# Kernel optimization log

Hardware: AMD Instinct MI355X
Metric: run time of the kernel (lower is better)

The kernel has to match this reference:

```python
import jax, jax.numpy as jnp
import numpy as np

C, H, D = 64, 2, 32
NQ, NA, NE, F_IN = 8192, 32768, 500000, 128
E_E2Q, E_E2E, E_E2A, E_Q2A = 131072, 800000, 262144, 32768
N_POS, N_NEG = 8192, 24576
# node types: 0=question, 1=answer, 2=entity
# edge types (src_type, dst_type): e2q=(2,0), e2e=(2,2), e2a=(2,1), q2a=(0,1)
REL_ST = [(2, 0), (2, 2), (2, 1), (0, 1)]


def _edges(k, n_src, n_dst, e):
    k1, k2 = jax.random.split(k)
    return jnp.stack([jax.random.randint(k1, (e,), 0, n_src),
                      jax.random.randint(k2, (e,), 0, n_dst)]).astype(jnp.int32)


def setup_inputs():
    key = jax.random.key(0)
    ks = jax.random.split(key, 16)
    inp = {
        'x_question': jax.random.normal(ks[0], (NQ, F_IN), jnp.float32),
        'x_answer': jax.random.normal(ks[1], (NA, F_IN), jnp.float32),
        'x_entity': jax.random.normal(ks[2], (NE, F_IN), jnp.float32),
        'e_e2q': _edges(ks[3], NE, NQ, E_E2Q),
        'e_e2e': _edges(ks[4], NE, NE, E_E2E),
        'e_e2a': _edges(ks[5], NE, NA, E_E2A),
        'e_q2a': _edges(ks[6], NQ, NA, E_Q2A),
        'pos_idx': _edges(ks[7], NQ, NA, N_POS),
        'neg_idx': _edges(ks[8], NQ, NA, N_NEG),
        # learned parameters (stacked over the 3 node types / 4 edge types)
        'W_in': jax.random.normal(ks[9], (3, F_IN, C), jnp.float32) / np.sqrt(F_IN).astype(np.float32),
        'b_in': jnp.zeros((3, C), jnp.float32),
        'bn_gamma': jnp.ones((3, C), jnp.float32),
        'bn_beta': jnp.zeros((3, C), jnp.float32),
        'W_kqv': jax.random.normal(ks[10], (3, C, 3 * C), jnp.float32) / np.sqrt(C).astype(np.float32),
        'b_kqv': jnp.zeros((3, 3 * C), jnp.float32),
        'A_k': jax.random.normal(ks[11], (4, H, D, D), jnp.float32) / np.sqrt(D).astype(np.float32),
        'A_v': jax.random.normal(ks[12], (4, H, D, D), jnp.float32) / np.sqrt(D).astype(np.float32),
        'p_rel': jnp.ones((4, H), jnp.float32),
        'W_out': jax.random.normal(ks[13], (3, C, C), jnp.float32) / np.sqrt(C).astype(np.float32),
        'b_out': jnp.zeros((3, C), jnp.float32),
        'skip': jnp.ones((3,), jnp.float32),
    }
    return inp


def _segment_attn(scores, vals, dst, n):
    # scores [E,H], vals [E,H,D]: softmax over incoming edges per dst node, weighted scatter-add
    m = jax.ops.segment_max(scores, dst, num_segments=n)          # [N,H]
    e = jnp.exp(scores - m[dst])                                   # [E,H]
    s = jax.ops.segment_sum(e, dst, num_segments=n)                # [N,H]
    w = e / s[dst]
    return jax.ops.segment_sum(vals * w[..., None], dst, num_segments=n)  # [N,H,D]


def _forward(x_question, x_answer, x_entity, W_in, b_in, bn_gamma, bn_beta,
             W_kqv, b_kqv, A_k, A_v, p_rel, W_out, b_out, skip, edges):
    xs = [x_question, x_answer, x_entity]
    h = []
    for t in range(3):
        y = jax.nn.relu(xs[t] @ W_in[t] + b_in[t])
        mu = y.mean(0)
        var = y.var(0)  # biased, as in torch BN training mode
        y = bn_gamma[t] * (y - mu) * jax.lax.rsqrt(var + 1e-5) + bn_beta[t]
        h.append(y)
    kqv = [h[t] @ W_kqv[t] + b_kqv[t] for t in range(3)]
    k = [kv[:, :C].reshape(-1, H, D) for kv in kqv]
    q = [kv[:, C:2 * C].reshape(-1, H, D) for kv in kqv]
    v = [kv[:, 2 * C:].reshape(-1, H, D) for kv in kqv]
    by_dst = {0: [], 1: [], 2: []}
    inv_sqrt_d = jnp.float32(1.0 / np.sqrt(D))
    for r, ((st, dt), ei) in enumerate(zip(REL_ST, edges)):
        src, dst = ei[0], ei[1]
        k_r = jnp.einsum('ehd,hdf->ehf', k[st][src], A_k[r])   # per-relation key transform
        v_r = jnp.einsum('ehd,hdf->ehf', v[st][src], A_v[r])   # per-relation value transform
        sc = (q[dt][dst] * k_r).sum(-1) * p_rel[r] * inv_sqrt_d  # [E,H]
        by_dst[dt].append((sc, v_r, dst))
    out = []
    for t in range(3):
        sc = jnp.concatenate([a for a, _, _ in by_dst[t]], axis=0)
        vr = jnp.concatenate([b for _, b, _ in by_dst[t]], axis=0)
        dst = jnp.concatenate([c for _, _, c in by_dst[t]], axis=0)
        n = h[t].shape[0]
        agg = _segment_attn(sc, vr, dst, n).reshape(n, C)
        a = jax.nn.gelu(agg, approximate=False) @ W_out[t] + b_out[t]
        g = jax.nn.sigmoid(skip[t])
        out.append(g * a + (1.0 - g) * h[t])
    return out  # [z_question, z_answer, z_entity]


def reference(x_question, x_answer, x_entity, e_e2q, e_e2e, e_e2a, e_q2a,
              pos_idx, neg_idx, W_in, b_in, bn_gamma, bn_beta, W_kqv, b_kqv,
              A_k, A_v, p_rel, W_out, b_out, skip):
    zq, za, ze = _forward(x_question, x_answer, x_entity, W_in, b_in, bn_gamma,
                          bn_beta, W_kqv, b_kqv, A_k, A_v, p_rel, W_out, b_out,
                          skip, [e_e2q, e_e2e, e_e2a, e_q2a])
    pos_pred = (zq[pos_idx[0]] * za[pos_idx[1]]).sum(-1)
    neg_pred = (zq[neg_idx[0]] * za[neg_idx[1]]).sum(-1)
    return pos_pred, neg_pred, zq, za, ze
```

## Files before the change

### kernel.cpp

```cpp
#include <hip/hip_runtime.h>
#include <hip/hip_bf16.h>
#include <hip/hip_fp16.h>
#include <math.h>

#define NQ 8192
#define NA 32768
#define NE 500000
#define F_IN 128
#define E_E2Q 131072
#define E_E2E 800000
#define E_E2A 262144
#define E_Q2A 32768
#define N_POS 8192
#define N_NEG 24576

#define NT_TOTAL (NQ + NA + NE)
#define E_TOTAL (E_E2Q + E_E2E + E_E2A + E_Q2A)
#define NBLK_SCAN ((NT_TOTAL + 1023) / 1024)
#define CDIV(a, b) (((a) + (b) - 1) / (b))

#define BASE_Q 0
#define BASE_A NQ
#define BASE_E (NQ + NA)

#define GIN_Q 128
#define GIN_A 512
#define GIN_E 768
#define GIN_TOT (GIN_Q + GIN_A + GIN_E)
#define HB 1024

#define GB_Q 2048
#define GB_E 4096
#define GB_A 8192

#define TOP_Q 64
#define TOP_A 256
#define TOP_E 3907

#define KQ_Q 32
#define KQ_E 1954
#define KQ_A 128
#define KQ_TOT (KQ_Q + 2 * KQ_E + KQ_A)
#define SCB 2048
#define SMEM_KQV 64512

typedef _Float16 half8_t __attribute__((ext_vector_type(8)));
typedef _Float16 half2_t __attribute__((ext_vector_type(2)));
typedef float f32x4_t __attribute__((ext_vector_type(4)));

__device__ inline void load_lds16(const void* g, void* l) {
  __builtin_amdgcn_global_load_lds((const __attribute__((address_space(1))) void*)g,
                                   (__attribute__((address_space(3))) void*)l, 16, 0, 0);
}

__device__ inline float fast_gelu(float v) {
  float u = 1.5957691216057308f * fmaf(0.044715f * v * v, v, v);
  return v / (1.f + __expf(-u));
}


__global__ __launch_bounds__(256) void prep_misc(
    float* __restrict__ row_start_f,
    const float* __restrict__ W_in, _Float16* __restrict__ WinT,
    const float* __restrict__ W_out, _Float16* __restrict__ WoutT)
{
  int bid = blockIdx.x;
  if (bid < 128) {
    size_t i = (size_t)bid * 256 + threadIdx.x;
    size_t stride = (size_t)128 * 256;
    for (; i < NT_TOTAL; i += stride) row_start_f[i] = 0.f;
  } else if (bid < 320) {
    int b = bid - 128;
    int t = b >> 6, n = b & 63, k = threadIdx.x;
    if (k < 136) {
      float v = (k < 128) ? W_in[(size_t)t * 128 * 64 + (size_t)k * 64 + n] : 0.f;
      WinT[((size_t)t * 64 + n) * 136 + k] = (_Float16)v;
    }
  } else {
    int b = bid - 320;
    int t = b >> 6, n = b & 63, k = threadIdx.x;
    if (k < 72) {
      float v = (k < 64) ? W_out[(size_t)t * 64 * 64 + (size_t)k * 64 + n] : 0.f;
      WoutT[((size_t)t * 64 + n) * 72 + k] = (_Float16)v;
    }
  }
}


__global__ __launch_bounds__(256) void inproj_hist_all(
    const float* __restrict__ xq, const float* __restrict__ xa,
    const float* __restrict__ xe,
    const _Float16* __restrict__ WinT, const float* __restrict__ b_in,
    _Float16* __restrict__ y_h, float* __restrict__ bstats,
    const int* __restrict__ hd0, const int* __restrict__ hd1,
    const int* __restrict__ hd2, const int* __restrict__ hd3,
    unsigned* __restrict__ cnt)
{
  __shared__ __align__(16) float bufA[32 * 128];
  __shared__ __align__(16) float bufB[32 * 128];
  __shared__ _Float16 Bs[64 * 136];
  __shared__ float s1[64], s2[64];

  int bid = blockIdx.x;
  if (bid >= GIN_TOT) {
    int i = (bid - GIN_TOT) * 256 + threadIdx.x;
    int stride = HB * 256;
    for (; i < E_TOTAL; i += stride) {
      if (i < E_E2Q) atomicAdd(&cnt[BASE_Q + hd0[i]], 1u);
      else if (i < E_E2Q + E_E2E) atomicAdd(&cnt[BASE_E + hd1[i - E_E2Q]], 1u);
      else if (i < E_E2Q + E_E2E + E_E2A)
        atomicAdd(&cnt[BASE_A + hd2[i - E_E2Q - E_E2E]], 1u);
      else atomicAdd(&cnt[BASE_A + hd3[i - E_E2Q - E_E2E - E_E2A]], 1u);
    }
    return;
  }

  int t, lb, nb;
  const float* Af;
  _Float16* oh;
  if (bid < GIN_Q)              { t = 0; lb = bid;                 nb = GIN_Q; Af = xq; oh = y_h; }
  else if (bid < GIN_Q + GIN_A) { t = 1; lb = bid - GIN_Q;         nb = GIN_A; Af = xa; oh = y_h + (size_t)NQ * 64; }
  else                          { t = 2; lb = bid - GIN_Q - GIN_A; nb = GIN_E; Af = xe; oh = y_h + (size_t)(NQ + NA) * 64; }
  int M = (t == 0) ? NQ : (t == 1) ? NA : NE;
  int nh = CDIV(M, 32);
  const _Float16* WT = WinT + (size_t)t * 64 * 136;
  const float* bias = b_in + t * 64;

  int tid = threadIdx.x, w = tid >> 6, l = tid & 63;
  int lr = l & 15, lg = l >> 4;
  int wrow = (w & 1) * 16;
  int wcol = (w >> 1) * 32;

  for (int idx = tid; idx < 64 * 136 / 8; idx += 256)
    *(half8_t*)&Bs[idx * 8] = *(const half8_t*)&WT[(size_t)idx * 8];
  if (tid < 64) { s1[tid] = 0.f; s2[tid] = 0.f; }

  float bval[2];
  bval[0] = bias[wcol + lr];
  bval[1] = bias[wcol + 16 + lr];
  float ps1[2] = {}, ps2[2] = {};

  auto stage = [&](float* buf, int h) {
    const char* srcbase = (const char*)Af + (size_t)h * 32 * 512;
    int rowlim = M - h * 32;
#pragma unroll
    for (int r = 0; r < 4; ++r) {
      int unit = r * 4 + w;
      char* ldst = (char*)buf + unit * 1024;
      int p = unit * 1024 + l * 16;
      int row = p >> 9;
      const char* src = (row < rowlim) ? srcbase + (size_t)row * 512 + (p & 511)
                                       : srcbase;
      load_lds16(src, ldst);
    }
  };

  int h0 = lb;
  if (h0 < nh) stage(bufA, h0);
  __syncthreads();

  float* cur = bufA;
  float* nxt = bufB;
  for (int h = h0; h < nh; h += nb) {
    int h2 = h + nb;
    bool more = h2 < nh;
    if (more) {
      stage(nxt, h2);
      asm volatile("s_waitcnt vmcnt(4)" ::: "memory");
    } else {
      asm volatile("s_waitcnt vmcnt(0)" ::: "memory");
    }
    __builtin_amdgcn_sched_barrier(0);
    __builtin_amdgcn_s_barrier();

    f32x4_t acc[2] = {};
#pragma unroll
    for (int ks = 0; ks < 4; ++ks) {
      const float4* pa = (const float4*)((const char*)cur +
                          (wrow + lr) * 512 + ks * 128 + lg * 32);
      float4 x0 = pa[0], x1 = pa[1];
      half8_t a0 = {(_Float16)x0.x, (_Float16)x0.y, (_Float16)x0.z, (_Float16)x0.w,
                    (_Float16)x1.x, (_Float16)x1.y, (_Float16)x1.z, (_Float16)x1.w};
#pragma unroll
      for (int ct = 0; ct < 2; ++ct) {
        half8_t b = *(const half8_t*)&Bs[(wcol + ct * 16 + lr) * 136 + ks * 32 + lg * 8];
        acc[ct] = __builtin_amdgcn_mfma_f32_16x16x32_f16(a0, b, acc[ct], 0, 0, 0);
      }
    }
    int rbase = h * 32 + wrow + lg * 4;
#pragma unroll
    for (int ct = 0; ct < 2; ++ct) {
      int col = wcol + ct * 16 + lr;
#pragma unroll
      for (int j = 0; j < 4; ++j) {
        int row = rbase + j;
        if (row >= M) continue;
        float val = fmaxf(acc[ct][j] + bval[ct], 0.f);
        oh[(size_t)row * 64 + col] = (_Float16)val;
        ps1[ct] += val;
        ps2[ct] += val * val;
      }
    }
    __builtin_amdgcn_s_barrier();
    float* tmp = cur; cur = nxt; nxt = tmp;
  }

#pragma unroll
  for (int ct = 0; ct < 2; ++ct) {
    int col = wcol + ct * 16 + lr;
    atomicAdd(&s1[col], ps1[ct]);
    atomicAdd(&s2[col], ps2[ct]);
  }
  __syncthreads();
  if (tid < 64) {
    bstats[(size_t)blockIdx.x * 128 + tid] = s1[tid];
    bstats[(size_t)blockIdx.x * 128 + 64 + tid] = s2[tid];
  }
}


__global__ __launch_bounds__(256) void reduce_scan1(
    const float* __restrict__ bstats, float* __restrict__ stats,
    unsigned* __restrict__ arr, unsigned* __restrict__ bsums)
{
  __shared__ __align__(16) char shbuf[1024];
  int bid = blockIdx.x;
  int t0 = threadIdx.x;
  if (bid < 384) {
    float* sh = (float*)shbuf;
    int t = bid >> 7, c = bid & 127;
    int nb = (t == 0) ? GIN_Q : (t == 1) ? GIN_A : GIN_E;
    int base = (t == 0) ? 0 : (t == 1) ? GIN_Q : (GIN_Q + GIN_A);
    float s = 0.f;
    for (int i = t0; i < nb; i += 256)
      s += bstats[(size_t)(base + i) * 128 + c];
    sh[t0] = s;
    __syncthreads();
    for (int off2 = 128; off2 > 0; off2 >>= 1) {
      if (t0 < off2) sh[t0] += sh[t0 + off2];
      __syncthreads();
    }
    if (t0 == 0) stats[t * 128 + c] = sh[0];
  } else {
    unsigned* sh = (unsigned*)shbuf;
    int blk = bid - 384;
    int base = blk * 1024 + t0 * 4;
    unsigned v[4];
    unsigned s = 0;
#pragma unroll
    for (int j = 0; j < 4; ++j) {
      v[j] = (base + j < NT_TOTAL) ? arr[base + j] : 0u;
      s += v[j];
    }
    sh[t0] = s;
    __syncthreads();
    for (int off = 1; off < 256; off <<= 1) {
      unsigned x = (t0 >= off) ? sh[t0 - off] : 0u;
      __syncthreads();
      sh[t0] += x;
      __syncthreads();
    }
    unsigned run = sh[t0] - s;
#pragma unroll
    for (int j = 0; j < 4; ++j) {
      if (base + j < NT_TOTAL) arr[base + j] = run;
      run += v[j];
    }
    if (t0 == 255) bsums[blk] = sh[255];
  }
}


__global__ __launch_bounds__(256) void scan2_bn(
    unsigned* __restrict__ bsums, int nbk,
    const float* __restrict__ stats,
    const float* __restrict__ gamma, const float* __restrict__ beta,
    float* __restrict__ scale, float* __restrict__ shift,
    const float* __restrict__ b_kqv, const float* __restrict__ W_kqv,
    float* __restrict__ bias2)
{
  int t0 = threadIdx.x;
  if (blockIdx.x == 0) {
    __shared__ unsigned sh[256];
    __shared__ unsigned carry;
    if (t0 == 0) carry = 0;
    __syncthreads();
    for (int chunk = 0; chunk < nbk; chunk += 256) {
      int i = chunk + t0;
      unsigned v = (i < nbk) ? bsums[i] : 0u;
      sh[t0] = v;
      __syncthreads();
      for (int off = 1; off < 256; off <<= 1) {
        unsigned x = (t0 >= off) ? sh[t0 - off] : 0u;
        __syncthreads();
        sh[t0] += x;
        __syncthreads();
      }
      unsigned inc = sh[t0];
      unsigned c = carry;
      __syncthreads();
      if (i < nbk) bsums[i] = c + inc - v;
      if (t0 == 255) carry = c + sh[255];
      __syncthreads();
    }
  } else {
    __shared__ float sshift[192];
    if (t0 < 192) {
      int ty = t0 >> 6, c = t0 & 63;
      float invN = (ty == 0) ? (1.f / NQ) : (ty == 1) ? (1.f / NA) : (1.f / NE);
      float mu = stats[ty * 128 + c] * invN;
      float var = stats[ty * 128 + 64 + c] * invN - mu * mu;
      float rs = rsqrtf(var + 1e-5f);
      float gm = gamma[t0];
      float sc = gm * rs;
      float sf = beta[t0] - gm * mu * rs;
      scale[t0] = sc;
      shift[t0] = sf;
      sshift[t0] = sf;
    }
    __syncthreads();
    for (int idx = t0; idx < 576; idx += 256) {
      int t = idx / 192, n = idx % 192;
      float s = b_kqv[t * 192 + n];
      for (int k = 0; k < 64; ++k)
        s += sshift[t * 64 + k] * W_kqv[(size_t)t * 64 * 192 + k * 192 + n];
      bias2[t * 192 + n] = s;
    }
  }
}


__global__ __launch_bounds__(256) void scan3_wprep(
    unsigned* __restrict__ arr, const unsigned* __restrict__ bsums,
    unsigned* __restrict__ cursor,
    const float* __restrict__ W_kqv, const float* __restrict__ bias2,
    const float* __restrict__ A_k, const float* __restrict__ A_v,
    const float* __restrict__ scale,
    _Float16* __restrict__ WqT, _Float16* __restrict__ WeT,
    _Float16* __restrict__ WaT, float* __restrict__ bias_big)
{
  int bid = blockIdx.x;
  int t0 = threadIdx.x;
  if (bid < NBLK_SCAN) {
    int base = bid * 1024 + t0 * 4;
    unsigned add = bsums[bid];
#pragma unroll
    for (int j = 0; j < 4; ++j) {
      int idx = base + j;
      if (idx < NT_TOTAL) {
        unsigned r = arr[idx] + add;
        arr[idx] = r;
        cursor[idx] = r;
      }
    }
    return;
  }
  int j = (bid - NBLK_SCAN) * 4 + (t0 >> 6);
  int c = t0 & 63;
  if (j >= 640) return;
  int t, jj, bofs;
  _Float16* W;
  if (j < 192)      { t = 0; jj = j;       W = WqT; bofs = 0; }
  else if (j < 512) { t = 2; jj = j - 192; W = WeT; bofs = 192; }
  else              { t = 1; jj = j - 512; W = WaT; bofs = 512; }
  const float* Wt = W_kqv + (size_t)t * 64 * 192;
  const float* b2 = bias2 + t * 192;
  int mode = 0, rel = 0, sub = 0;
  if (t == 1) { mode = 1; rel = (jj < 64) ? 2 : 3; sub = jj & 63; }
  else if (jj >= 64 && jj < 128) { mode = 1; rel = (t == 0) ? 0 : 1; sub = jj - 64; }
  else if (jj >= 128) {
    mode = 2; sub = (jj - 128) & 63;
    rel = (t == 0) ? 3 : ((jj - 128) >> 6);
  }
  int h = sub >> 5, x = sub & 31;
  float wv, bv;
  if (mode == 0) {
    wv = Wt[(size_t)c * 192 + jj];
    bv = b2[jj];
  } else if (mode == 1) {
    const float* Ar = A_k + ((size_t)rel * 2048 + h * 1024 + x * 32);
    float s = 0.f, sb = 0.f;
    for (int f = 0; f < 32; ++f) {
      float a = Ar[f];
      s = fmaf(a, Wt[(size_t)c * 192 + 64 + h * 32 + f], s);
      sb = fmaf(a, b2[64 + h * 32 + f], sb);
    }
    wv = s; bv = sb;
  } else {
    const float* Ar = A_v + ((size_t)rel * 2048 + h * 1024 + x);
    float s = 0.f, sb = 0.f;
    for (int d = 0; d < 32; ++d) {
      float a = Ar[d * 32];
      s = fmaf(a, Wt[(size_t)c * 192 + 128 + h * 32 + d], s);
      sb = fmaf(a, b2[128 + h * 32 + d], sb);
    }
    wv = s; bv = sb;
  }
  wv *= scale[t * 64 + c];
  W[(size_t)jj * 72 + c] = (_Float16)wv;
  if (c < 8) W[(size_t)jj * 72 + 64 + c] = (_Float16)0.f;
  if (c == 0) bias_big[bofs + jj] = bv;
}


template <int BNT>
__device__ __forceinline__ void kqv_body(
    char* smem,
    const _Float16* __restrict__ Ah,
    const _Float16* __restrict__ WT, const float* __restrict__ bias, int M,
    _Float16* __restrict__ oh, int LDO, int row0, int colbase)
{
  constexpr int KP = 72;
  constexpr int TP = BNT + 8;
  _Float16* As = (_Float16*)smem;
  _Float16* Bs = As + 256 * KP;
  _Float16* Ts = (_Float16*)smem;
  int tid = threadIdx.x;

  {
    for (int idx = tid; idx < 256 * 8; idx += 512) {
      int row = idx >> 3, c = (idx & 7);
      int gr = row0 + row;
      half8_t a8 = {};
      if (gr < M) a8 = *(const half8_t*)&Ah[(size_t)gr * 64 + c * 8];
      *(half8_t*)&As[row * KP + c * 8] = a8;
    }
  }
  {
    const _Float16* wsrc = WT + (size_t)colbase * KP;
    for (int idx = tid; idx < BNT * KP / 8; idx += 512)
      *(half8_t*)&Bs[idx * 8] = *(const half8_t*)&wsrc[(size_t)idx * 8];
  }
  __syncthreads();

  int w = tid >> 6, l = tid & 63;
  int lr = l & 15, lg = l >> 4;
  constexpr int NCT = BNT / 16;
  f32x4_t acc[2][NCT] = {};
#pragma unroll
  for (int ks = 0; ks < 2; ++ks) {
    half8_t a0 = *(const half8_t*)&As[(w * 32 + lr) * KP + ks * 32 + lg * 8];
    half8_t a1 = *(const half8_t*)&As[(w * 32 + 16 + lr) * KP + ks * 32 + lg * 8];
#pragma unroll
    for (int ct = 0; ct < NCT; ++ct) {
      half8_t b = *(const half8_t*)&Bs[(ct * 16 + lr) * KP + ks * 32 + lg * 8];
      acc[0][ct] = __builtin_amdgcn_mfma_f32_16x16x32_f16(a0, b, acc[0][ct], 0, 0, 0);
      acc[1][ct] = __builtin_amdgcn_mfma_f32_16x16x32_f16(a1, b, acc[1][ct], 0, 0, 0);
    }
  }

  float bval[NCT];
#pragma unroll
  for (int ct = 0; ct < NCT; ++ct) bval[ct] = bias[colbase + ct * 16 + lr];

#pragma unroll
  for (int rt = 0; rt < 2; ++rt) {
    __syncthreads();
    int r2base = w * 16 + lg * 4;
#pragma unroll
    for (int ct = 0; ct < NCT; ++ct) {
      int colL = ct * 16 + lr;
#pragma unroll
      for (int j = 0; j < 4; ++j)
        Ts[(r2base + j) * TP + colL] = (_Float16)(acc[rt][ct][j] + bval[ct]);
    }
    __syncthreads();
    constexpr int C8 = BNT / 8;
    for (int idx = tid; idx < 128 * C8; idx += 512) {
      int r2 = idx / C8, c8 = (idx % C8) * 8;
      int gr = row0 + (r2 >> 4) * 32 + rt * 16 + (r2 & 15);
      if (gr < M)
        *(half8_t*)&oh[(size_t)gr * LDO + colbase + c8] = *(const half8_t*)&Ts[r2 * TP + c8];
    }
  }
}


__global__ __launch_bounds__(512) void kqv_scatter(
    const _Float16* __restrict__ y_h,
    const _Float16* __restrict__ WqT, const _Float16* __restrict__ WeT,
    const _Float16* __restrict__ WaT, const float* __restrict__ bias_big,
    _Float16* __restrict__ kqvQ, _Float16* __restrict__ kqvE,
    _Float16* __restrict__ kqvA,
    const int* __restrict__ s0, const int* __restrict__ d0,
    const int* __restrict__ s1, const int* __restrict__ d1,
    const int* __restrict__ s2, const int* __restrict__ d2,
    const int* __restrict__ s3, const int* __restrict__ d3,
    unsigned* __restrict__ cursor, unsigned* __restrict__ eidx)
{
  extern __shared__ __align__(16) char smem[];
  int bid = blockIdx.x;
  if (bid < KQ_Q) {
    kqv_body<192>(smem, y_h, WqT, bias_big, NQ, kqvQ, 192, bid * 256, 0);
  } else if (bid < KQ_Q + 2 * KQ_E) {
    int b = bid - KQ_Q;
    int ct = b / KQ_E;
    int rb = b % KQ_E;
    kqv_body<160>(smem, y_h + (size_t)(NQ + NA) * 64, WeT, bias_big + 192, NE,
                  kqvE, 320, rb * 256, ct * 160);
  } else if (bid < KQ_TOT) {
    int b = bid - KQ_Q - 2 * KQ_E;
    kqv_body<128>(smem, y_h + (size_t)NQ * 64, WaT, bias_big + 512, NA,
                  kqvA, 128, b * 256, 0);
  } else {
    int i = (bid - KQ_TOT) * 512 + threadIdx.x;
    int stride = SCB * 512;
    for (; i < E_TOTAL; i += stride) {
      unsigned pos, pay;
      if (i < E_E2Q) {
        pos = atomicAdd(&cursor[BASE_Q + d0[i]], 1u);
        pay = (unsigned)(s0[i] * 320);
      } else if (i < E_E2Q + E_E2E) {
        int k = i - E_E2Q;
        pos = atomicAdd(&cursor[BASE_E + d1[k]], 1u);
        pay = (unsigned)(s1[k] * 320);
      } else if (i < E_E2Q + E_E2E + E_E2A) {
        int k = i - E_E2Q - E_E2E;
        pos = atomicAdd(&cursor[BASE_A + d2[k]], 1u);
        pay = (unsigned)(s2[k] * 320);
      } else {
        int k = i - E_E2Q - E_E2E - E_E2A;
        pos = atomicAdd(&cursor[BASE_A + d3[k]], 1u);
        pay = (unsigned)(s3[k] * 192) | 0x80000000u;
      }
      eidx[pos] = pay;
    }
  }
}


template <int NREL>
__device__ __forceinline__ void gather_body(
    int bidLocal, int nblocks, int N, int nodebase,
    const unsigned* __restrict__ row_start, const unsigned* __restrict__ row_end,
    const unsigned* __restrict__ eidx,
    const _Float16* __restrict__ baseA, int vofA,
    const _Float16* __restrict__ baseB, int vofB,
    const _Float16* __restrict__ qtA, int ldqA,
    const _Float16* __restrict__ qtB, int ldqB,
    const float* __restrict__ prelA, const float* __restrict__ prelB,
    _Float16* __restrict__ agg)
{
  int lane = threadIdx.x & 63;
  int h = lane >> 5, f = lane & 31;
  int idx2 = h * 32 + 2 * (f & 15);
  const float isd = 0.17677669529663687f;
  float pr0 = prelA[h] * isd;
  float pr1 = (NREL == 2) ? prelB[h] * isd : 0.f;

  int wid = (int)(((size_t)bidLocal * 256 + threadIdx.x) >> 6);
  int nw = nblocks * 4;

  int n0 = wid;
  unsigned b0s = 0, b0e = 0, e00 = 0, e01 = 0;
  half2_t q00p = {}, q01p = {};
  if (n0 < N) {
    b0s = row_start[nodebase + n0];
    b0e = row_end[nodebase + n0];
    q00p = *(const half2_t*)&qtA[(size_t)n0 * ldqA + idx2];
    if (NREL == 2) q01p = *(const half2_t*)&qtB[(size_t)n0 * ldqB + idx2];
    e00 = eidx[b0s];
    e01 = eidx[b0s + 1];
  }
  int n1 = n0 + nw;
  unsigned b1s = 0, b1e = 0;
  half2_t q10p = {}, q11p = {};
  if (n0 < N && n1 < N) {
    b1s = row_start[nodebase + n1];
    b1e = row_end[nodebase + n1];
    q10p = *(const half2_t*)&qtA[(size_t)n1 * ldqA + idx2];
    if (NREL == 2) q11p = *(const half2_t*)&qtB[(size_t)n1 * ldqB + idx2];
  }

  while (n0 < N) {
    unsigned e10 = 0, e11 = 0;
    if (n1 < N) {
      e10 = eidx[b1s];
      e11 = eidx[b1s + 1];
    }
    int n2 = n1 + nw;
    unsigned b2s = 0, b2e = 0;
    half2_t q20p = {}, q21p = {};
    if (n2 < N) {
      b2s = row_start[nodebase + n2];
      b2e = row_end[nodebase + n2];
      q20p = *(const half2_t*)&qtA[(size_t)n2 * ldqA + idx2];
      if (NREL == 2) q21p = *(const half2_t*)&qtB[(size_t)n2 * ldqB + idx2];
    }

    float vs = 0.f, ss = 0.f;
    unsigned i = b0s;

    auto do_pair = [&](unsigned p1, unsigned p2) {
      unsigned o1 = p1 & 0x7FFFFFFFu, o2 = p2 & 0x7FFFFFFFu;
      bool r1 = (NREL == 2) && (p1 >> 31);
      bool r2 = (NREL == 2) && (p2 >> 31);
      const _Float16* b1 = (r1 ? baseB : baseA) + o1;
      const _Float16* b2 = (r2 ? baseB : baseA) + o2;
      half2_t k21 = *(const half2_t*)&b1[idx2];
      float v1 = (float)b1[(r1 ? vofB : vofA) + lane];
      half2_t k22 = *(const half2_t*)&b2[idx2];
      float v2 = (float)b2[(r2 ? vofB : vofA) + lane];
      float sa = __builtin_amdgcn_fdot2(k21, r1 ? q01p : q00p, 0.f, false);
      float sb = __builtin_amdgcn_fdot2(k22, r2 ? q01p : q00p, 0.f, false);
#pragma unroll
      for (int off = 1; off <= 8; off <<= 1) {
        sa += __shfl_xor(sa, off, 32);
        sb += __shfl_xor(sb, off, 32);
      }
      float w1 = __expf(sa * (r1 ? pr1 : pr0));
      float w2 = __expf(sb * (r2 ? pr1 : pr0));
      ss += w1 + w2;
      vs = fmaf(w1, v1, vs);
      vs = fmaf(w2, v2, vs);
    };
    auto do_single = [&](unsigned p1) {
      unsigned o1 = p1 & 0x7FFFFFFFu;
      bool r1 = (NREL == 2) && (p1 >> 31);
      const _Float16* b1 = (r1 ? baseB : baseA) + o1;
      half2_t k21 = *(const half2_t*)&b1[idx2];
      float v1 = (float)b1[(r1 ? vofB : vofA) + lane];
      float sa = __builtin_amdgcn_fdot2(k21, r1 ? q01p : q00p, 0.f, false);
#pragma unroll
      for (int off = 1; off <= 8; off <<= 1) sa += __shfl_xor(sa, off, 32);
      float w1 = __expf(sa * (r1 ? pr1 : pr0));
      ss += w1;
      vs = fmaf(w1, v1, vs);
    };

    if (i + 2 <= b0e) { do_pair(e00, e01); i += 2; }
    else if (i < b0e) { do_single(e00); i = b0e; }
    for (; i + 2 <= b0e; i += 2) do_pair(eidx[i], eidx[i + 1]);
    if (i < b0e) do_single(eidx[i]);

    float val = (ss > 0.f) ? vs / ss : 0.f;
    val = fast_gelu(val);
    agg[((size_t)(nodebase + n0)) * 64 + lane] = (_Float16)val;

    n0 = n1; b0s = b1s; b0e = b1e; q00p = q10p; q01p = q11p; e00 = e10; e01 = e11;
    n1 = n2; b1s = b2s; b1e = b2e; q10p = q20p; q11p = q21p;
  }
}

__global__ __launch_bounds__(256) void gather_all(
    const unsigned* __restrict__ row_start, const unsigned* __restrict__ row_end,
    const unsigned* __restrict__ eidx,
    const _Float16* __restrict__ kqvQ, const _Float16* __restrict__ kqvE,
    const _Float16* __restrict__ kqvA,
    const float* __restrict__ p_rel, _Float16* __restrict__ agg)
{
  int bid = blockIdx.x;
  if (bid < GB_Q) {
    gather_body<1>(bid, GB_Q, NQ, BASE_Q, row_start, row_end, eidx,
                   kqvE, 128, kqvE, 128, kqvQ + 64, 192, kqvQ + 64, 192,
                   p_rel + 0, p_rel + 0, agg);
  } else if (bid < GB_Q + GB_E) {
    gather_body<1>(bid - GB_Q, GB_E, NE, BASE_E, row_start, row_end, eidx,
                   kqvE, 192, kqvE, 192, kqvE + 64, 320, kqvE + 64, 320,
                   p_rel + 2, p_rel + 2, agg);
  } else {
    gather_body<2>(bid - GB_Q - GB_E, GB_A, NA, BASE_A, row_start, row_end, eidx,
                   kqvE, 256, kqvQ, 128, kqvA, 128, kqvA + 64, 128,
                   p_rel + 4, p_rel + 6, agg);
  }
}


__global__ __launch_bounds__(256) void gemm_out_all(
    const _Float16* __restrict__ agg_h, const _Float16* __restrict__ y_h,
    const _Float16* __restrict__ WoutT, const float* __restrict__ b_out,
    const float* __restrict__ scale, const float* __restrict__ shift,
    const float* __restrict__ skip, float* __restrict__ zout)
{
  __shared__ _Float16 Bs[64 * 72];
  int bid = blockIdx.x;
  int t, row0, M;
  size_t nodeoff;
  if (bid < TOP_Q)              { t = 0; row0 = bid * 128;              M = NQ; nodeoff = 0; }
  else if (bid < TOP_Q + TOP_A) { t = 1; row0 = (bid - TOP_Q) * 128;    M = NA; nodeoff = NQ; }
  else                          { t = 2; row0 = (bid - TOP_Q - TOP_A) * 128; M = NE; nodeoff = NQ + NA; }
  const _Float16* Ah = agg_h + nodeoff * 64;
  const _Float16* resh = y_h + nodeoff * 64;
  float* Cf = zout + nodeoff * 64;
  const _Float16* WT = WoutT + (size_t)t * 64 * 72;
  const float* bias = b_out + t * 64;
  const float* rsc = scale + t * 64;
  const float* rsh = shift + t * 64;

  int tid = threadIdx.x;
  int w = tid >> 6, l = tid & 63;
  int lr = l & 15, lg = l >> 4;

  for (int idx = tid; idx < 64 * 72 / 8; idx += 256)
    *(half8_t*)&Bs[idx * 8] = *(const half8_t*)&WT[(size_t)idx * 8];

  half8_t afrag[2][2];
#pragma unroll
  for (int rt = 0; rt < 2; ++rt) {
    int gr = row0 + w * 32 + rt * 16 + lr;
    bool ok = gr < M;
#pragma unroll
    for (int ks = 0; ks < 2; ++ks) {
      half8_t h8 = {};
      if (ok) h8 = *(const half8_t*)&Ah[(size_t)gr * 64 + ks * 32 + lg * 8];
      afrag[rt][ks] = h8;
    }
  }
  __syncthreads();

  f32x4_t acc[2][4] = {};
#pragma unroll
  for (int ks = 0; ks < 2; ++ks) {
#pragma unroll
    for (int ct = 0; ct < 4; ++ct) {
      half8_t b = *(const half8_t*)&Bs[(ct * 16 + lr) * 72 + ks * 32 + lg * 8];
      acc[0][ct] = __builtin_amdgcn_mfma_f32_16x16x32_f16(afrag[0][ks], b, acc[0][ct], 0, 0, 0);
      acc[1][ct] = __builtin_amdgcn_mfma_f32_16x16x32_f16(afrag[1][ks], b, acc[1][ct], 0, 0, 0);
    }
  }

  float g = 1.f / (1.f + __expf(-skip[t]));
  float gb = 1.f - g;
#pragma unroll
  for (int rt = 0; rt < 2; ++rt) {
    int rbase = row0 + w * 32 + rt * 16 + lg * 4;
#pragma unroll
    for (int ct = 0; ct < 4; ++ct) {
      int col = ct * 16 + lr;
      float bval = bias[col];
#pragma unroll
      for (int j = 0; j < 4; ++j) {
        int row = rbase + j;
        if (row >= M) continue;
        float val = acc[rt][ct][j] + bval;
        float rv = (float)resh[(size_t)row * 64 + col];
        Cf[(size_t)row * 64 + col] = g * val + gb * (rsc[col] * rv + rsh[col]);
      }
    }
  }
}


__global__ void pred_all(const int* __restrict__ pos, const int* __restrict__ neg,
                         const float* __restrict__ zq, const float* __restrict__ za,
                         float* __restrict__ outp) {
  int i = blockIdx.x * blockDim.x + threadIdx.x;
  if (i >= N_POS + N_NEG) return;
  int k; const int* qi; const int* ai; float* o;
  if (i < N_POS) { k = i; qi = pos; ai = pos + N_POS; o = outp; }
  else { k = i - N_POS; qi = neg; ai = neg + N_NEG; o = outp + N_POS; }
  const float4* a = (const float4*)(zq + (size_t)qi[k] * 64);
  const float4* b = (const float4*)(za + (size_t)ai[k] * 64);
  float ssum = 0.f;
#pragma unroll
  for (int j = 0; j < 16; ++j) {
    float4 x = a[j], y = b[j];
    ssum += x.x * y.x + x.y * y.y + x.z * y.z + x.w * y.w;
  }
  o[k] = ssum;
}


extern "C" void kernel_launch(void* const* d_in, const int* in_sizes, int n_in,
                              void* d_out, int out_size, void* d_ws, size_t ws_size,
                              hipStream_t stream) {
  const float* xq = (const float*)d_in[0];
  const float* xa = (const float*)d_in[1];
  const float* xe = (const float*)d_in[2];
  const int* e_e2q = (const int*)d_in[3];
  const int* e_e2e = (const int*)d_in[4];
  const int* e_e2a = (const int*)d_in[5];
  const int* e_q2a = (const int*)d_in[6];
  const int* pos_idx = (const int*)d_in[7];
  const int* neg_idx = (const int*)d_in[8];
  const float* W_in = (const float*)d_in[9];
  const float* b_in = (const float*)d_in[10];
  const float* bn_gamma = (const float*)d_in[11];
  const float* bn_beta = (const float*)d_in[12];
  const float* W_kqv = (const float*)d_in[13];
  const float* b_kqv = (const float*)d_in[14];
  const float* A_k = (const float*)d_in[15];
  const float* A_v = (const float*)d_in[16];
  const float* p_rel = (const float*)d_in[17];
  const float* W_out = (const float*)d_in[18];
  const float* b_out = (const float*)d_in[19];
  const float* skip = (const float*)d_in[20];
  float* out = (float*)d_out;

  float* ws = (float*)d_ws;
  size_t off = 0;
  _Float16* y_h = (_Float16*)(ws + off);    off += (size_t)NT_TOTAL * 32;
  _Float16* kqvQ = (_Float16*)(ws + off);   off += (size_t)NQ * 96;
  _Float16* kqvE = (_Float16*)(ws + off);   off += (size_t)NE * 160;
  _Float16* kqvA = (_Float16*)(ws + off);   off += (size_t)NA * 64;
  _Float16* agg_h = (_Float16*)(ws + off);  off += (size_t)NT_TOTAL * 32;
  float* stats = ws + off;                  off += 384;
  float* scale = ws + off;                  off += 192;
  float* shift = ws + off;                  off += 192;
  float* bias2 = ws + off;                  off += 576;
  float* bias_big = ws + off;               off += 640;
  _Float16* WqT = (_Float16*)(ws + off);    off += 192 * 72 / 2;
  _Float16* WeT = (_Float16*)(ws + off);    off += 320 * 72 / 2;
  _Float16* WaT = (_Float16*)(ws + off);    off += 128 * 72 / 2;
  _Float16* WinT = (_Float16*)(ws + off);   off += 3 * 64 * 136 / 2;
  _Float16* WoutT = (_Float16*)(ws + off);  off += 3 * 64 * 72 / 2;
  float* bstats = ws + off;                 off += (size_t)GIN_TOT * 128;
  unsigned* row_start = (unsigned*)(ws + off); off += NT_TOTAL;
  unsigned* cursor = (unsigned*)(ws + off);    off += NT_TOTAL;
  unsigned* bsums = (unsigned*)(ws + off);     off += 1024;
  unsigned* eidx = (unsigned*)(ws + off);      off += E_TOTAL + 8;

  float* zq_out = out + (N_POS + N_NEG);

  prep_misc<<<dim3(512), dim3(256), 0, stream>>>((float*)row_start, W_in, WinT, W_out, WoutT);

  inproj_hist_all<<<dim3(GIN_TOT + HB), dim3(256), 0, stream>>>(
      xq, xa, xe, WinT, b_in, y_h, bstats,
      e_e2q + E_E2Q, e_e2e + E_E2E, e_e2a + E_E2A, e_q2a + E_Q2A, row_start);

  reduce_scan1<<<dim3(384 + NBLK_SCAN), dim3(256), 0, stream>>>(
      bstats, stats, row_start, bsums);

  scan2_bn<<<dim3(2), dim3(256), 0, stream>>>(
      bsums, NBLK_SCAN, stats, bn_gamma, bn_beta, scale, shift, b_kqv, W_kqv, bias2);

  scan3_wprep<<<dim3(NBLK_SCAN + 160), dim3(256), 0, stream>>>(
      row_start, bsums, cursor, W_kqv, bias2, A_k, A_v, scale,
      WqT, WeT, WaT, bias_big);

  kqv_scatter<<<dim3(KQ_TOT + SCB), dim3(512), SMEM_KQV, stream>>>(
      y_h, WqT, WeT, WaT, bias_big, kqvQ, kqvE, kqvA,
      e_e2q, e_e2q + E_E2Q, e_e2e, e_e2e + E_E2E,
      e_e2a, e_e2a + E_E2A, e_q2a, e_q2a + E_Q2A, cursor, eidx);

  gather_all<<<dim3(GB_Q + GB_E + GB_A), dim3(256), 0, stream>>>(
      row_start, cursor, eidx, kqvQ, kqvE, kqvA, p_rel, agg_h);

  gemm_out_all<<<dim3(TOP_Q + TOP_A + TOP_E), dim3(256), 0, stream>>>(
      agg_h, y_h, WoutT, b_out, scale, shift, skip, zq_out);

  pred_all<<<dim3(CDIV(N_POS + N_NEG, 256)), dim3(256), 0, stream>>>(
      pos_idx, neg_idx, zq_out, zq_out + (size_t)NQ * 64, out);
}
```

Baseline: 655.1 us.

## Shrink KQV GEMM tiles to 128 rows and reorder scatter blocks first

```diff
diff --git a/kernel.cpp b/kernel.cpp
--- a/kernel.cpp
+++ b/kernel.cpp
@@ -37,12 +37,12 @@
 #define TOP_A 256
 #define TOP_E 3907
 
-#define KQ_Q 32
-#define KQ_E 1954
-#define KQ_A 128
-#define KQ_TOT (KQ_Q + 2 * KQ_E + KQ_A)
 #define SCB 2048
-#define SMEM_KQV 64512
+#define KQ2_Q 64
+#define KQ2_E 3907
+#define KQ2_A 256
+#define KS2_TOT (SCB + KQ2_Q + 2 * KQ2_E + KQ2_A)
+#define SMEM_KQV2 51200
 
 typedef _Float16 half8_t __attribute__((ext_vector_type(8)));
 typedef _Float16 half2_t __attribute__((ext_vector_type(2)));
@@ -404,7 +404,7 @@
 
 
 template <int BNT>
-__device__ __forceinline__ void kqv_body(
+__device__ __forceinline__ void kqv_body128(
     char* smem,
     const _Float16* __restrict__ Ah,
     const _Float16* __restrict__ WT, const float* __restrict__ bias, int M,
@@ -413,22 +413,20 @@
   constexpr int KP = 72;
   constexpr int TP = BNT + 8;
   _Float16* As = (_Float16*)smem;
-  _Float16* Bs = As + 256 * KP;
+  _Float16* Bs = As + 128 * KP;
   _Float16* Ts = (_Float16*)smem;
   int tid = threadIdx.x;
 
-  {
-    for (int idx = tid; idx < 256 * 8; idx += 512) {
-      int row = idx >> 3, c = (idx & 7);
-      int gr = row0 + row;
-      half8_t a8 = {};
-      if (gr < M) a8 = *(const half8_t*)&Ah[(size_t)gr * 64 + c * 8];
-      *(half8_t*)&As[row * KP + c * 8] = a8;
-    }
+  for (int idx = tid; idx < 128 * 8; idx += 256) {
+    int row = idx >> 3, c = idx & 7;
+    int gr = row0 + row;
+    half8_t a8 = {};
+    if (gr < M) a8 = *(const half8_t*)&Ah[(size_t)gr * 64 + c * 8];
+    *(half8_t*)&As[row * KP + c * 8] = a8;
   }
   {
     const _Float16* wsrc = WT + (size_t)colbase * KP;
-    for (int idx = tid; idx < BNT * KP / 8; idx += 512)
+    for (int idx = tid; idx < BNT * KP / 8; idx += 256)
       *(half8_t*)&Bs[idx * 8] = *(const half8_t*)&wsrc[(size_t)idx * 8];
   }
   __syncthreads();
@@ -453,10 +451,10 @@
 #pragma unroll
   for (int ct = 0; ct < NCT; ++ct) bval[ct] = bias[colbase + ct * 16 + lr];
 
+  __syncthreads();
 #pragma unroll
   for (int rt = 0; rt < 2; ++rt) {
-    __syncthreads();
-    int r2base = w * 16 + lg * 4;
+    int r2base = w * 32 + rt * 16 + lg * 4;
 #pragma unroll
     for (int ct = 0; ct < NCT; ++ct) {
       int colL = ct * 16 + lr;
@@ -464,19 +462,19 @@
       for (int j = 0; j < 4; ++j)
         Ts[(r2base + j) * TP + colL] = (_Float16)(acc[rt][ct][j] + bval[ct]);
     }
-    __syncthreads();
-    constexpr int C8 = BNT / 8;
-    for (int idx = tid; idx < 128 * C8; idx += 512) {
-      int r2 = idx / C8, c8 = (idx % C8) * 8;
-      int gr = row0 + (r2 >> 4) * 32 + rt * 16 + (r2 & 15);
-      if (gr < M)
-        *(half8_t*)&oh[(size_t)gr * LDO + colbase + c8] = *(const half8_t*)&Ts[r2 * TP + c8];
-    }
-  }
-}
-
-
-__global__ __launch_bounds__(512) void kqv_scatter(
+  }
+  __syncthreads();
+  constexpr int C8 = BNT / 8;
+  for (int idx = tid; idx < 128 * C8; idx += 256) {
+    int r2 = idx / C8, c8 = (idx % C8) * 8;
+    int gr = row0 + r2;
+    if (gr < M)
+      *(half8_t*)&oh[(size_t)gr * LDO + colbase + c8] = *(const half8_t*)&Ts[r2 * TP + c8];
+  }
+}
+
+
+__global__ __launch_bounds__(256) void kqv_scatter2(
     const _Float16* __restrict__ y_h,
     const _Float16* __restrict__ WqT, const _Float16* __restrict__ WeT,
     const _Float16* __restrict__ WaT, const float* __restrict__ bias_big,
@@ -490,21 +488,9 @@
 {
   extern __shared__ __align__(16) char smem[];
   int bid = blockIdx.x;
-  if (bid < KQ_Q) {
-    kqv_body<192>(smem, y_h, WqT, bias_big, NQ, kqvQ, 192, bid * 256, 0);
-  } else if (bid < KQ_Q + 2 * KQ_E) {
-    int b = bid - KQ_Q;
-    int ct = b / KQ_E;
-    int rb = b % KQ_E;
-    kqv_body<160>(smem, y_h + (size_t)(NQ + NA) * 64, WeT, bias_big + 192, NE,
-                  kqvE, 320, rb * 256, ct * 160);
-  } else if (bid < KQ_TOT) {
-    int b = bid - KQ_Q - 2 * KQ_E;
-    kqv_body<128>(smem, y_h + (size_t)NQ * 64, WaT, bias_big + 512, NA,
-                  kqvA, 128, b * 256, 0);
-  } else {
-    int i = (bid - KQ_TOT) * 512 + threadIdx.x;
-    int stride = SCB * 512;
+  if (bid < SCB) {
+    int i = bid * 256 + threadIdx.x;
+    int stride = SCB * 256;
     for (; i < E_TOTAL; i += stride) {
       unsigned pos, pay;
       if (i < E_E2Q) {
@@ -525,6 +511,19 @@
       }
       eidx[pos] = pay;
     }
+  } else if (bid < SCB + 2 * KQ2_E) {
+    int b = bid - SCB;
+    int ct = b / KQ2_E;
+    int rb = b % KQ2_E;
+    kqv_body128<160>(smem, y_h + (size_t)(NQ + NA) * 64, WeT, bias_big + 192, NE,
+                     kqvE, 320, rb * 128, ct * 160);
+  } else if (bid < SCB + 2 * KQ2_E + KQ2_Q) {
+    int b = bid - SCB - 2 * KQ2_E;
+    kqv_body128<192>(smem, y_h, WqT, bias_big, NQ, kqvQ, 192, b * 128, 0);
+  } else {
+    int b = bid - SCB - 2 * KQ2_E - KQ2_Q;
+    kqv_body128<128>(smem, y_h + (size_t)NQ * 64, WaT, bias_big + 512, NA,
+                     kqvA, 128, b * 128, 0);
   }
 }
 
@@ -828,7 +827,7 @@
       row_start, bsums, cursor, W_kqv, bias2, A_k, A_v, scale,
       WqT, WeT, WaT, bias_big);
 
-  kqv_scatter<<<dim3(KQ_TOT + SCB), dim3(512), SMEM_KQV, stream>>>(
+  kqv_scatter2<<<dim3(KS2_TOT), dim3(256), SMEM_KQV2, stream>>>(
       y_h, WqT, WeT, WaT, bias_big, kqvQ, kqvE, kqvA,
       e_e2q, e_e2q + E_E2Q, e_e2e, e_e2e + E_E2E,
       e_e2a, e_e2a + E_E2A, e_q2a, e_q2a + E_Q2A, cursor, eidx);
```

Result: no change. 662.0 us (+1.0%).

## Shrink KQV GEMM tiles and load A fragments directly into registers

Applied to the files above, without the earlier changes.

```diff
diff --git a/kernel.cpp b/kernel.cpp
--- a/kernel.cpp
+++ b/kernel.cpp
@@ -37,12 +37,12 @@
 #define TOP_A 256
 #define TOP_E 3907
 
-#define KQ_Q 32
-#define KQ_E 1954
-#define KQ_A 128
-#define KQ_TOT (KQ_Q + 2 * KQ_E + KQ_A)
+#define KQ3_E 3907
+#define KQ3_Q 64
+#define KQ3_A 256
 #define SCB 2048
-#define SMEM_KQV 64512
+#define KS3_TOT (2 * KQ3_E + 2 * KQ3_Q + KQ3_A + SCB)
+#define SMEM_KQV3 43008
 
 typedef _Float16 half8_t __attribute__((ext_vector_type(8)));
 typedef _Float16 half2_t __attribute__((ext_vector_type(2)));
@@ -404,7 +404,7 @@
 
 
 template <int BNT>
-__device__ __forceinline__ void kqv_body(
+__device__ __forceinline__ void kqv_bodyD(
     char* smem,
     const _Float16* __restrict__ Ah,
     const _Float16* __restrict__ WT, const float* __restrict__ bias, int M,
@@ -412,71 +412,73 @@
 {
   constexpr int KP = 72;
   constexpr int TP = BNT + 8;
-  _Float16* As = (_Float16*)smem;
-  _Float16* Bs = As + 256 * KP;
+  constexpr int NCTW = BNT / 32;
+  _Float16* Bs = (_Float16*)smem;
   _Float16* Ts = (_Float16*)smem;
   int tid = threadIdx.x;
-
-  {
-    for (int idx = tid; idx < 256 * 8; idx += 512) {
-      int row = idx >> 3, c = (idx & 7);
-      int gr = row0 + row;
-      half8_t a8 = {};
-      if (gr < M) a8 = *(const half8_t*)&Ah[(size_t)gr * 64 + c * 8];
-      *(half8_t*)&As[row * KP + c * 8] = a8;
-    }
-  }
+  int w = tid >> 6, l = tid & 63;
+  int rw = w >> 1, cw = w & 1;
+  int lr = l & 15, lg = l >> 4;
+
   {
     const _Float16* wsrc = WT + (size_t)colbase * KP;
     for (int idx = tid; idx < BNT * KP / 8; idx += 512)
       *(half8_t*)&Bs[idx * 8] = *(const half8_t*)&wsrc[(size_t)idx * 8];
   }
+  half8_t afrag[2][2];
+#pragma unroll
+  for (int rt = 0; rt < 2; ++rt) {
+    int gr = row0 + rw * 32 + rt * 16 + lr;
+    bool ok = gr < M;
+#pragma unroll
+    for (int ks = 0; ks < 2; ++ks) {
+      half8_t h8 = {};
+      if (ok) h8 = *(const half8_t*)&Ah[(size_t)gr * 64 + ks * 32 + lg * 8];
+      afrag[rt][ks] = h8;
+    }
+  }
   __syncthreads();
 
-  int w = tid >> 6, l = tid & 63;
-  int lr = l & 15, lg = l >> 4;
-  constexpr int NCT = BNT / 16;
-  f32x4_t acc[2][NCT] = {};
+  f32x4_t acc[2][NCTW] = {};
 #pragma unroll
   for (int ks = 0; ks < 2; ++ks) {
-    half8_t a0 = *(const half8_t*)&As[(w * 32 + lr) * KP + ks * 32 + lg * 8];
-    half8_t a1 = *(const half8_t*)&As[(w * 32 + 16 + lr) * KP + ks * 32 + lg * 8];
-#pragma unroll
-    for (int ct = 0; ct < NCT; ++ct) {
-      half8_t b = *(const half8_t*)&Bs[(ct * 16 + lr) * KP + ks * 32 + lg * 8];
-      acc[0][ct] = __builtin_amdgcn_mfma_f32_16x16x32_f16(a0, b, acc[0][ct], 0, 0, 0);
-      acc[1][ct] = __builtin_amdgcn_mfma_f32_16x16x32_f16(a1, b, acc[1][ct], 0, 0, 0);
-    }
-  }
-
-  float bval[NCT];
-#pragma unroll
-  for (int ct = 0; ct < NCT; ++ct) bval[ct] = bias[colbase + ct * 16 + lr];
-
+#pragma unroll
+    for (int ct = 0; ct < NCTW; ++ct) {
+      half8_t b = *(const half8_t*)&Bs[(cw * (BNT / 2) + ct * 16 + lr) * KP + ks * 32 + lg * 8];
+      acc[0][ct] = __builtin_amdgcn_mfma_f32_16x16x32_f16(afrag[0][ks], b, acc[0][ct], 0, 0, 0);
+      acc[1][ct] = __builtin_amdgcn_mfma_f32_16x16x32_f16(afrag[1][ks], b, acc[1][ct], 0, 0, 0);
+    }
+  }
+
+  float bval[NCTW];
+#pragma unroll
+  for (int ct = 0; ct < NCTW; ++ct)
+    bval[ct] = bias[colbase + cw * (BNT / 2) + ct * 16 + lr];
+
+  __syncthreads();
 #pragma unroll
   for (int rt = 0; rt < 2; ++rt) {
-    __syncthreads();
-    int r2base = w * 16 + lg * 4;
-#pragma unroll
-    for (int ct = 0; ct < NCT; ++ct) {
-      int colL = ct * 16 + lr;
+    int r2base = rw * 32 + rt * 16 + lg * 4;
+#pragma unroll
+    for (int ct = 0; ct < NCTW; ++ct) {
+      int colL = cw * (BNT / 2) + ct * 16 + lr;
 #pragma unroll
       for (int j = 0; j < 4; ++j)
         Ts[(r2base + j) * TP + colL] = (_Float16)(acc[rt][ct][j] + bval[ct]);
     }
-    __syncthreads();
-    constexpr int C8 = BNT / 8;
-    for (int idx = tid; idx < 128 * C8; idx += 512) {
-      int r2 = idx / C8, c8 = (idx % C8) * 8;
-      int gr = row0 + (r2 >> 4) * 32 + rt * 16 + (r2 & 15);
-      if (gr < M)
-        *(half8_t*)&oh[(size_t)gr * LDO + colbase + c8] = *(const half8_t*)&Ts[r2 * TP + c8];
-    }
-  }
-}
-
-
-__global__ __launch_bounds__(512) void kqv_scatter(
+  }
+  __syncthreads();
+  constexpr int C8 = BNT / 8;
+  for (int idx = tid; idx < 128 * C8; idx += 512) {
+    int r2 = idx / C8, c8 = (idx % C8) * 8;
+    int gr = row0 + r2;
+    if (gr < M)
+      *(half8_t*)&oh[(size_t)gr * LDO + colbase + c8] = *(const half8_t*)&Ts[r2 * TP + c8];
+  }
+}
+
+
+__global__ __launch_bounds__(512) void kqv_scatter3(
     const _Float16* __restrict__ y_h,
     const _Float16* __restrict__ WqT, const _Float16* __restrict__ WeT,
     const _Float16* __restrict__ WaT, const float* __restrict__ bias_big,
@@ -490,20 +492,22 @@
 {
   extern __shared__ __align__(16) char smem[];
   int bid = blockIdx.x;
-  if (bid < KQ_Q) {
-    kqv_body<192>(smem, y_h, WqT, bias_big, NQ, kqvQ, 192, bid * 256, 0);
-  } else if (bid < KQ_Q + 2 * KQ_E) {
-    int b = bid - KQ_Q;
-    int ct = b / KQ_E;
-    int rb = b % KQ_E;
-    kqv_body<160>(smem, y_h + (size_t)(NQ + NA) * 64, WeT, bias_big + 192, NE,
-                  kqvE, 320, rb * 256, ct * 160);
-  } else if (bid < KQ_TOT) {
-    int b = bid - KQ_Q - 2 * KQ_E;
-    kqv_body<128>(smem, y_h + (size_t)NQ * 64, WaT, bias_big + 512, NA,
-                  kqvA, 128, b * 256, 0);
+  if (bid < 2 * KQ3_E) {
+    int ct = bid / KQ3_E;
+    int rb = bid % KQ3_E;
+    kqv_bodyD<160>(smem, y_h + (size_t)(NQ + NA) * 64, WeT, bias_big + 192, NE,
+                   kqvE, 320, rb * 128, ct * 160);
+  } else if (bid < 2 * KQ3_E + 2 * KQ3_Q) {
+    int b = bid - 2 * KQ3_E;
+    int ct = b / KQ3_Q;
+    int rb = b % KQ3_Q;
+    kqv_bodyD<96>(smem, y_h, WqT, bias_big, NQ, kqvQ, 192, rb * 128, ct * 96);
+  } else if (bid < 2 * KQ3_E + 2 * KQ3_Q + KQ3_A) {
+    int b = bid - 2 * KQ3_E - 2 * KQ3_Q;
+    kqv_bodyD<128>(smem, y_h + (size_t)NQ * 64, WaT, bias_big + 512, NA,
+                   kqvA, 128, b * 128, 0);
   } else {
-    int i = (bid - KQ_TOT) * 512 + threadIdx.x;
+    int i = (bid - 2 * KQ3_E - 2 * KQ3_Q - KQ3_A) * 512 + threadIdx.x;
     int stride = SCB * 512;
     for (; i < E_TOTAL; i += stride) {
       unsigned pos, pay;
@@ -828,7 +832,7 @@
       row_start, bsums, cursor, W_kqv, bias2, A_k, A_v, scale,
       WqT, WeT, WaT, bias_big);
 
-  kqv_scatter<<<dim3(KQ_TOT + SCB), dim3(512), SMEM_KQV, stream>>>(
+  kqv_scatter3<<<dim3(KS3_TOT), dim3(512), SMEM_KQV3, stream>>>(
       y_h, WqT, WeT, WaT, bias_big, kqvQ, kqvE, kqvA,
       e_e2q, e_e2q + E_E2Q, e_e2e, e_e2e + E_E2E,
       e_e2a, e_e2a + E_E2A, e_q2a, e_q2a + E_Q2A, cursor, eidx);
```

New measurement: 645.0 us. About the same (-1.5%).
